# Kernel tuning notes

Measured on AMD Instinct MI355X. Metric: run time of the kernel, lower is better.

## Reference

```python
import jax, jax.numpy as jnp
import numpy as np

HID = 384
KV = 384
HEADS = 2
LAYERS = 2
KFFN = 9
WIN = 0.2
SIGMA = 0.3
EPS = 1e-5
HDIM = HID // HEADS


def _sin_pos(T, dim):
    # fairseq SinusoidalPositionalEmbedding; inputs are nonzero floats so all
    # positions are "non-pad": positions = arange(T) + padding_idx + 1 = 1..T
    pos = jnp.arange(1, T + 1, dtype=jnp.float32)
    half = dim // 2
    freqs = jnp.exp(-np.log(10000.0) / (half - 1) * jnp.arange(half, dtype=jnp.float32))
    ang = pos[:, None] * freqs[None, :]
    return jnp.concatenate([jnp.sin(ang), jnp.cos(ang)], axis=-1)  # [T, dim]


def _ln(x, g, b):
    m = jnp.mean(x, axis=-1, keepdims=True)
    v = jnp.var(x, axis=-1, keepdims=True)
    return (x - m) * jax.lax.rsqrt(v + EPS) * g + b


def _window_mask(T1, T2):
    # per-query sliding window over keys (vectorized form of the Python loop)
    w = int(T2 * WIN) // 2
    t = jnp.arange(T1)
    c = (t * T2) // T1                      # win_center = int(t/T1*T2)
    lo = jnp.maximum(0, c - w)
    j = jnp.arange(T2)
    allowed = (j[None, :] >= lo[:, None]) & (j[None, :] < (c + w)[:, None])
    return ~allowed                          # True = masked out, [T1, T2]


def _forward(x1, x2, pos_alpha, ln1_g, ln1_b, qw, kw, vw, ow,
             ln2_g, ln2_b, cw, cb, lw, lb, lnf_g, lnf_b):
    B, T1, C = x1.shape
    T2 = x2.shape[1]
    # no padding (random-normal inputs never have zero abs-sum rows), so all
    # nonpadding multiplies are identity and key_padding_mask is a no-op.
    x1 = x1 + pos_alpha * _sin_pos(T1, C)[None]
    x2 = x2 + pos_alpha * _sin_pos(T2, KV)[None]

    mask = _window_mask(T1, T2)              # [T1, T2] bool
    scaling = HDIM ** -0.5
    guided_loss = jnp.float32(0.0)
    # guided attention mask (lengths == full lengths, no padding)
    ti = jnp.arange(T1, dtype=jnp.float32)[:, None] / T1
    sj = jnp.arange(T2, dtype=jnp.float32)[None, :] / T2
    gmask = 1.0 - jnp.exp(-((sj - ti) ** 2) / (2.0 * SIGMA ** 2))  # [T1, T2]

    aw = None
    for i in range(LAYERS):
        residual = x1
        qn = _ln(x1, ln1_g[i], ln1_b[i])
        q = jnp.einsum('btc,dc->btd', qn, qw[i]) * scaling
        k = jnp.einsum('bsc,dc->bsd', x2, kw[i])
        v = jnp.einsum('bsc,dc->bsd', x2, vw[i])
        q = q.reshape(B, T1, HEADS, HDIM)
        k = k.reshape(B, T2, HEADS, HDIM)
        v = v.reshape(B, T2, HEADS, HDIM)
        scores = jnp.einsum('bqhd,bkhd->bhqk', q, k)
        scores = jnp.where(mask[None, None], jnp.float32(-1e9), scores)
        p = jax.nn.softmax(scores, axis=-1)                  # [B,H,T1,T2]
        attn = jnp.einsum('bhqk,bkhd->bqhd', p, v).reshape(B, T1, C)
        attn = jnp.einsum('btc,dc->btd', attn, ow[i])
        x1 = residual + attn
        if i == 0:  # num_guided_layers = 1
            aw = p.mean(axis=1)                              # head-avg [B,T1,T2]
            guided_loss = guided_loss + (aw * gmask[None]).mean()
        # FFN: Conv1d(C->4C, k=9, SAME) * k^-0.5 -> gelu -> Linear(4C->C)
        residual = x1
        y = _ln(x1, ln2_g[i], ln2_b[i])
        yt = jnp.transpose(y, (0, 2, 1))                     # [B,C,T1]
        h = jax.lax.conv_general_dilated(yt, cw[i], (1,), 'SAME',
                                         dimension_numbers=('NCH', 'OIH', 'NCH'))
        h = (h + cb[i][None, :, None]) * (KFFN ** -0.5)
        h = jax.nn.gelu(jnp.transpose(h, (0, 2, 1)), approximate=False)  # [B,T1,4C]
        y = jnp.einsum('btf,cf->btc', h, lw[i]) + lb[i]
        x1 = residual + y

    x1 = _ln(x1, lnf_g, lnf_b)
    return x1, guided_loss


def setup_inputs() -> dict:
    key = jax.random.key(0)
    ks = jax.random.split(key, 16)
    s = 0.02
    B, T1, T2 = 8, 2048, 512
    return {
        'x1': jax.random.normal(ks[0], (B, T1, HID), jnp.float32),
        'x2': jax.random.normal(ks[1], (B, T2, KV), jnp.float32),
        'pos_alpha': jnp.float32(1.0),
        'ln1_g': jnp.ones((LAYERS, HID), jnp.float32),
        'ln1_b': jnp.zeros((LAYERS, HID), jnp.float32),
        'qw': jax.random.normal(ks[2], (LAYERS, HID, HID), jnp.float32) * s,
        'kw': jax.random.normal(ks[3], (LAYERS, HID, KV), jnp.float32) * s,
        'vw': jax.random.normal(ks[4], (LAYERS, HID, KV), jnp.float32) * s,
        'ow': jax.random.normal(ks[5], (LAYERS, HID, HID), jnp.float32) * s,
        'ln2_g': jnp.ones((LAYERS, HID), jnp.float32),
        'ln2_b': jnp.zeros((LAYERS, HID), jnp.float32),
        'cw': jax.random.normal(ks[6], (LAYERS, 4 * HID, HID, KFFN), jnp.float32) * s,
        'cb': jnp.zeros((LAYERS, 4 * HID), jnp.float32),
        'lw': jax.random.normal(ks[7], (LAYERS, HID, 4 * HID), jnp.float32) * s,
        'lb': jnp.zeros((LAYERS, HID), jnp.float32),
        'lnf_g': jnp.ones((HID,), jnp.float32),
        'lnf_b': jnp.zeros((HID,), jnp.float32),
    }


def reference(x1, x2, pos_alpha, ln1_g, ln1_b, qw, kw, vw, ow,
              ln2_g, ln2_b, cw, cb, lw, lb, lnf_g, lnf_b):
    return _forward(x1, x2, pos_alpha, ln1_g, ln1_b, qw, kw, vw, ow,
                    ln2_g, ln2_b, cw, cb, lw, lb, lnf_g, lnf_b)
```

## Files before the change

### kernel.cpp

```cpp
#include <hip/hip_runtime.h>
#include <math.h>

#define NB 8
#define NT1 2048
#define NT2 512
#define NC 384
#define ND 192
#define NF 1536
#define NKI 3456
#define TPAD 2056

typedef __attribute__((ext_vector_type(8))) short bf16x8;
typedef __attribute__((ext_vector_type(4))) float f32x4;

#define GLOAD16(gsrc, ldst) \
  __builtin_amdgcn_global_load_lds((const __attribute__((address_space(1))) void*)(gsrc), \
                                   (__attribute__((address_space(3))) void*)(ldst), 16, 0, 0)

static __device__ __forceinline__ unsigned short f2bf(float f) {
  unsigned int u = __float_as_uint(f);
  unsigned int r = (u + 0x7fffu + ((u >> 16) & 1u)) >> 16;
  return (unsigned short)r;
}

static __device__ __forceinline__ float warp_sum(float v) {
#pragma unroll
  for (int off = 32; off > 0; off >>= 1) v += __shfl_xor(v, off);
  return v;
}

__global__ __launch_bounds__(256) void k_add_pos2(const float* __restrict__ x,
    const float* __restrict__ alpha_p, float* __restrict__ y, int T, int total2) {
  int i = blockIdx.x * 256 + threadIdx.x;
  if (i >= total2) return;
  int j = i % 192;
  int row = i / 192;
  int t = row % T;
  float freq = __expf(-0.0482216773f * (float)j);
  float ang = (float)(t + 1) * freq;
  float sn, cs;
  __sincosf(ang, &sn, &cs);
  float a = alpha_p[0];
  size_t base = (size_t)row * NC;
  y[base + j] = x[base + j] + a * sn;
  y[base + j + 192] = x[base + j + 192] + a * cs;
}

__global__ __launch_bounds__(256) void k_add_pos2_bf16(const float* __restrict__ x,
    const float* __restrict__ alpha_p, unsigned short* __restrict__ y, int T, int total2) {
  int i = blockIdx.x * 256 + threadIdx.x;
  if (i >= total2) return;
  int j = i % 192;
  int row = i / 192;
  int t = row % T;
  float freq = __expf(-0.0482216773f * (float)j);
  float ang = (float)(t + 1) * freq;
  float sn, cs;
  __sincosf(ang, &sn, &cs);
  float a = alpha_p[0];
  size_t base = (size_t)row * NC;
  y[base + j] = f2bf(x[base + j] + a * sn);
  y[base + j + 192] = f2bf(x[base + j + 192] + a * cs);
}

__global__ __launch_bounds__(256) void k_ln(const float* __restrict__ x,
    const float* __restrict__ g, const float* __restrict__ b,
    float* __restrict__ y, int nrows) {
  int row = blockIdx.x * 4 + (threadIdx.x >> 6);
  int lane = threadIdx.x & 63;
  if (row >= nrows) return;
  const float* xr = x + (size_t)row * NC;
  float v[6];
  float s = 0.f, s2 = 0.f;
#pragma unroll
  for (int i = 0; i < 6; ++i) {
    float t = xr[lane + 64 * i];
    v[i] = t; s += t; s2 += t * t;
  }
  s = warp_sum(s); s2 = warp_sum(s2);
  float mean = s * (1.f / NC);
  float var = s2 * (1.f / NC) - mean * mean;
  float rs = rsqrtf(var + 1e-5f);
  float* yr = y + (size_t)row * NC;
#pragma unroll
  for (int i = 0; i < 6; ++i) {
    int cc = lane + 64 * i;
    yr[cc] = (v[i] - mean) * rs * g[cc] + b[cc];
  }
}

__global__ __launch_bounds__(256) void k_ln_bf16(const float* __restrict__ x,
    const float* __restrict__ g, const float* __restrict__ b,
    unsigned short* __restrict__ y) {
  int row = blockIdx.x * 4 + (threadIdx.x >> 6);
  int lane = threadIdx.x & 63;
  const float* xr = x + (size_t)row * NC;
  float v[6];
  float s = 0.f, s2 = 0.f;
#pragma unroll
  for (int i = 0; i < 6; ++i) {
    float t = xr[lane + 64 * i];
    v[i] = t; s += t; s2 += t * t;
  }
  s = warp_sum(s); s2 = warp_sum(s2);
  float mean = s * (1.f / NC);
  float var = s2 * (1.f / NC) - mean * mean;
  float rs = rsqrtf(var + 1e-5f);
  unsigned short* yr = y + (size_t)row * NC;
#pragma unroll
  for (int i = 0; i < 6; ++i) {
    int cc = lane + 64 * i;
    yr[cc] = f2bf((v[i] - mean) * rs * g[cc] + b[cc]);
  }
}

__global__ __launch_bounds__(256) void k_ln_bf16p(const float* __restrict__ x,
    const float* __restrict__ g, const float* __restrict__ b,
    unsigned short* __restrict__ ypad) {
  int row = blockIdx.x * 4 + (threadIdx.x >> 6);
  int lane = threadIdx.x & 63;
  const float* xr = x + (size_t)row * NC;
  float v[6];
  float s = 0.f, s2 = 0.f;
#pragma unroll
  for (int i = 0; i < 6; ++i) {
    float t = xr[lane + 64 * i];
    v[i] = t; s += t; s2 += t * t;
  }
  s = warp_sum(s); s2 = warp_sum(s2);
  float mean = s * (1.f / NC);
  float var = s2 * (1.f / NC) - mean * mean;
  float rs = rsqrtf(var + 1e-5f);
  int bb = row >> 11, t = row & 2047;
  unsigned short* yr = ypad + ((size_t)(bb * TPAD + t + 4)) * NC;
#pragma unroll
  for (int i = 0; i < 6; ++i) {
    int cc = lane + 64 * i;
    yr[cc] = f2bf((v[i] - mean) * rs * g[cc] + b[cc]);
  }
}

__global__ __launch_bounds__(256) void k_zero_guard(unsigned short* __restrict__ ypad) {
  int i = blockIdx.x * 256 + threadIdx.x;
  if (i >= 24576) return;
  int c = i % NC;
  int r = (i / NC) % 8;
  int b = i / (NC * 8);
  int t = (r < 4) ? r : (2048 + r);
  ypad[((size_t)b * TPAD + t) * NC + c] = 0;
}

__global__ __launch_bounds__(256) void k_pack_cw2(const float* __restrict__ cw,
    unsigned short* __restrict__ cwp) {
  __shared__ float s[NKI];
  int f = blockIdx.x;
  const float* src = cw + (size_t)f * NKI;
  for (int i = threadIdx.x; i < NKI; i += 256) s[i] = src[i];
  __syncthreads();
  unsigned short* dst = cwp + (size_t)f * NKI;
  for (int i = threadIdx.x; i < NKI; i += 256) {
    int kk = i / NC, cc = i - kk * NC;
    dst[i] = f2bf(s[cc * 9 + kk]);
  }
}

__global__ __launch_bounds__(256) void k_cvt_scale(const float* __restrict__ x,
    unsigned short* __restrict__ y, int n, float scale) {
  int i = blockIdx.x * 256 + threadIdx.x;
  if (i < n) y[i] = f2bf(x[i] * scale);
}

__global__ __launch_bounds__(256) void k_pgemm_mfma(
    const unsigned short* __restrict__ A,
    const unsigned short* __restrict__ W,
    unsigned short* __restrict__ Cb,
    float* __restrict__ Cf,
    int K, int mode) {
  __shared__ unsigned short As[128 * 32];
  __shared__ unsigned short Bs[128 * 32];
  const int bn = blockIdx.x * 128;
  const int bm = blockIdx.y * 128;
  const int tid = threadIdx.x;
  const int lane = tid & 63, wv = tid >> 6;
  const int wr = (wv >> 1) * 64, wc = (wv & 1) * 64;
  f32x4 acc[4][4] = {};

  const int chunk = wv * 2;
  const int rloc = chunk * 16 + (lane >> 2);
  const int slot = (lane & 3) * 8;
  const size_t abase = ((size_t)(bm + rloc)) * K + slot;
  const size_t bbase = ((size_t)(bn + rloc)) * K + slot;
  unsigned short* AsW0 = &As[chunk * 512];
  unsigned short* AsW1 = &As[(chunk + 1) * 512];
  unsigned short* BsW0 = &Bs[chunk * 512];
  unsigned short* BsW1 = &Bs[(chunk + 1) * 512];

  const int rsel = lane & 15, ksel = (lane >> 4) * 8;

  for (int kt = 0; kt < K; kt += 32) {
    GLOAD16(A + abase + kt, AsW0);
    GLOAD16(A + abase + kt + (size_t)16 * K, AsW1);
    GLOAD16(W + bbase + kt, BsW0);
    GLOAD16(W + bbase + kt + (size_t)16 * K, BsW1);
    __syncthreads();
    bf16x8 af[4], bfr[4];
#pragma unroll
    for (int m = 0; m < 4; ++m)
      af[m] = *(const bf16x8*)&As[(wr + m * 16 + rsel) * 32 + ksel];
#pragma unroll
    for (int n = 0; n < 4; ++n)
      bfr[n] = *(const bf16x8*)&Bs[(wc + n * 16 + rsel) * 32 + ksel];
#pragma unroll
    for (int m = 0; m < 4; ++m)
#pragma unroll
      for (int n = 0; n < 4; ++n)
        acc[m][n] = __builtin_amdgcn_mfma_f32_16x16x32_bf16(af[m], bfr[n], acc[m][n], 0, 0, 0);
    __syncthreads();
  }

  const int col0 = bn + wc + (lane & 15);
  const int row0 = bm + wr + (lane >> 4) * 4;
#pragma unroll
  for (int m = 0; m < 4; ++m) {
#pragma unroll
    for (int n = 0; n < 4; ++n) {
      int col = col0 + n * 16;
#pragma unroll
      for (int r = 0; r < 4; ++r) {
        int row = row0 + m * 16 + r;
        if (mode == 0) {
          Cb[(size_t)row * NC + col] = f2bf(acc[m][n][r]);
        } else if (mode == 1) {
          size_t oi = (size_t)row * NC + col;
          Cf[oi] = acc[m][n][r] + Cf[oi];
        } else {
          Cb[((size_t)((row >> 9) * 384 + col)) * 512 + (row & 511)] = f2bf(acc[m][n][r]);
        }
      }
    }
  }
}

__global__ __launch_bounds__(512) void k_conv_mfma(
    const unsigned short* __restrict__ Ypad,
    const unsigned short* __restrict__ Wp,
    const float* __restrict__ cb,
    unsigned short* __restrict__ H) {
  __shared__ unsigned short As[2][256 * 64];
  __shared__ unsigned short Bs[2][128 * 64];
  const int bm = blockIdx.x * 256;
  const int bn = blockIdx.y * 128;
  const int b = bm >> 11, t0 = bm & 2047;
  const int tid = threadIdx.x;
  const int lane = tid & 63, wv = tid >> 6;
  const int wvM = wv >> 1, wvN = wv & 1;
  const int rsel = lane & 15, ghi = lane >> 4;
  const int l8 = lane >> 3, g8 = lane & 7;
  const int gsrc = (g8 ^ l8) * 8;

  f32x4 acc[4][4] = {};

  const size_t arow0 = (size_t)(b * TPAD + t0 + wv * 32 + l8);
  const size_t brow0 = (size_t)(bn + wv * 16 + l8);

#define CONV_STAGE(T, DB)                                                     \
  {                                                                           \
    const int kt_ = (T) * 64;                                                 \
    const int kk_ = kt_ / NC;                                                 \
    const int c0_ = kt_ - kk_ * NC;                                           \
    const size_t asrc_ = (arow0 + kk_) * NC + c0_ + gsrc;                     \
    GLOAD16(Ypad + asrc_, &As[DB][(wv * 32) * 64]);                           \
    GLOAD16(Ypad + asrc_ + (size_t)8 * NC, &As[DB][(wv * 32 + 8) * 64]);      \
    GLOAD16(Ypad + asrc_ + (size_t)16 * NC, &As[DB][(wv * 32 + 16) * 64]);    \
    GLOAD16(Ypad + asrc_ + (size_t)24 * NC, &As[DB][(wv * 32 + 24) * 64]);    \
    const size_t bsrc_ = brow0 * NKI + kt_ + gsrc;                            \
    GLOAD16(Wp + bsrc_, &Bs[DB][(wv * 16) * 64]);                             \
    GLOAD16(Wp + bsrc_ + (size_t)8 * NKI, &Bs[DB][(wv * 16 + 8) * 64]);       \
  }

  CONV_STAGE(0, 0);
  CONV_STAGE(1, 1);
  asm volatile("s_waitcnt vmcnt(6)" ::: "memory");
  __builtin_amdgcn_sched_barrier(0);
  __builtin_amdgcn_s_barrier();

  const int arow = wvM * 64;
  const int brow = wvN * 64;
  int db = 0;
  for (int t = 0; t < 54; ++t) {
    bf16x8 af[4][2], bfr[4][2];
#pragma unroll
    for (int m = 0; m < 4; ++m) {
      int r = arow + m * 16 + rsel;
#pragma unroll
      for (int k = 0; k < 2; ++k)
        af[m][k] = *(const bf16x8*)&As[db][r * 64 + (((k * 4 + ghi) ^ (r & 7)) * 8)];
    }
#pragma unroll
    for (int n = 0; n < 4; ++n) {
      int r = brow + n * 16 + rsel;
#pragma unroll
      for (int k = 0; k < 2; ++k)
        bfr[n][k] = *(const bf16x8*)&Bs[db][r * 64 + (((k * 4 + ghi) ^ (r & 7)) * 8)];
    }
    __builtin_amdgcn_s_setprio(1);
#pragma unroll
    for (int m = 0; m < 4; ++m)
#pragma unroll
      for (int n = 0; n < 4; ++n)
        acc[m][n] = __builtin_amdgcn_mfma_f32_16x16x32_bf16(af[m][0], bfr[n][0], acc[m][n], 0, 0, 0);
    __builtin_amdgcn_s_setprio(0);
    __builtin_amdgcn_sched_barrier(0);
    asm volatile("s_waitcnt lgkmcnt(0)" ::: "memory");
    __builtin_amdgcn_sched_barrier(0);
    __builtin_amdgcn_s_barrier();
    if (t + 2 < 54) CONV_STAGE(t + 2, db);
    __builtin_amdgcn_s_setprio(1);
#pragma unroll
    for (int m = 0; m < 4; ++m)
#pragma unroll
      for (int n = 0; n < 4; ++n)
        acc[m][n] = __builtin_amdgcn_mfma_f32_16x16x32_bf16(af[m][1], bfr[n][1], acc[m][n], 0, 0, 0);
    __builtin_amdgcn_s_setprio(0);
    __builtin_amdgcn_sched_barrier(0);
    if (t + 2 < 54) {
      asm volatile("s_waitcnt vmcnt(6)" ::: "memory");
    } else {
      asm volatile("s_waitcnt vmcnt(0)" ::: "memory");
    }
    __builtin_amdgcn_sched_barrier(0);
    __builtin_amdgcn_s_barrier();
    db ^= 1;
  }
#undef CONV_STAGE

  const int col0 = bn + wvN * 64 + rsel;
  const int row0 = bm + wvM * 64 + ghi * 4;
#pragma unroll
  for (int m = 0; m < 4; ++m) {
#pragma unroll
    for (int n = 0; n < 4; ++n) {
      int col = col0 + n * 16;
      float cbv = cb[col];
#pragma unroll
      for (int r = 0; r < 4; ++r) {
        int row = row0 + m * 16 + r;
        float xv = (acc[m][n][r] + cbv) * 0.33333333333333333f;
        float ge = 0.5f * xv * (1.f + erff(xv * 0.70710678118654752f));
        H[(size_t)row * NF + col] = f2bf(ge);
      }
    }
  }
}

__global__ __launch_bounds__(256) void k_lin_mfma(
    const unsigned short* __restrict__ H,
    const unsigned short* __restrict__ Wb,
    const float* __restrict__ lb,
    float* __restrict__ x1a) {
  __shared__ unsigned short As[128 * 32];
  __shared__ unsigned short Bs[128 * 32];
  const int bn = blockIdx.x * 128;
  const int bm = blockIdx.y * 128;
  const int tid = threadIdx.x;
  const int lane = tid & 63, wv = tid >> 6;
  const int wr = (wv >> 1) * 64, wc = (wv & 1) * 64;
  f32x4 acc[4][4] = {};

  const int chunk = wv * 2;
  const int rloc = chunk * 16 + (lane >> 2);
  const int slot = (lane & 3) * 8;
  const size_t abase = ((size_t)(bm + rloc)) * NF + slot;
  const size_t bbase = ((size_t)(bn + rloc)) * NF + slot;
  unsigned short* AsW0 = &As[chunk * 512];
  unsigned short* AsW1 = &As[(chunk + 1) * 512];
  unsigned short* BsW0 = &Bs[chunk * 512];
  unsigned short* BsW1 = &Bs[(chunk + 1) * 512];

  const int rsel = lane & 15, ksel = (lane >> 4) * 8;

  for (int kt = 0; kt < NF; kt += 32) {
    GLOAD16(H + abase + kt, AsW0);
    GLOAD16(H + abase + kt + (size_t)16 * NF, AsW1);
    GLOAD16(Wb + bbase + kt, BsW0);
    GLOAD16(Wb + bbase + kt + (size_t)16 * NF, BsW1);
    __syncthreads();
    bf16x8 af[4], bfr[4];
#pragma unroll
    for (int m = 0; m < 4; ++m)
      af[m] = *(const bf16x8*)&As[(wr + m * 16 + rsel) * 32 + ksel];
#pragma unroll
    for (int n = 0; n < 4; ++n)
      bfr[n] = *(const bf16x8*)&Bs[(wc + n * 16 + rsel) * 32 + ksel];
#pragma unroll
    for (int m = 0; m < 4; ++m)
#pragma unroll
      for (int n = 0; n < 4; ++n)
        acc[m][n] = __builtin_amdgcn_mfma_f32_16x16x32_bf16(af[m], bfr[n], acc[m][n], 0, 0, 0);
    __syncthreads();
  }

  const int col0 = bn + wc + (lane & 15);
  const int row0 = bm + wr + (lane >> 4) * 4;
#pragma unroll
  for (int m = 0; m < 4; ++m) {
#pragma unroll
    for (int n = 0; n < 4; ++n) {
      int col = col0 + n * 16;
      float lbv = lb[col];
#pragma unroll
      for (int r = 0; r < 4; ++r) {
        int row = row0 + m * 16 + r;
        size_t oi = (size_t)row * NC + col;
        x1a[oi] = acc[m][n][r] + lbv + x1a[oi];
      }
    }
  }
}

__global__ __launch_bounds__(256) void k_attn_mfma(
    const unsigned short* __restrict__ qbb,
    const unsigned short* __restrict__ kbb,
    const unsigned short* __restrict__ vtb,
    unsigned short* __restrict__ o, int guided, float* __restrict__ gl) {
  __shared__ unsigned short lds[32768];
  const int tid = threadIdx.x;
  const int lane = tid & 63, wv = tid >> 6;
  const int rsel = lane & 15, ghi = lane >> 4;
  const int idx = blockIdx.x;
  const int tg = idx & 31;
  const int bh = idx >> 5;
  const int h = bh & 1, b = bh >> 1;
  const int t0 = tg * 64;
  const int c0 = t0 >> 2;
  int klo = c0 - 51; if (klo < 0) klo = 0;
  klo &= ~7;
  if (klo > 384) klo = 384;

  const unsigned short* qrow = qbb + (size_t)(b * NT1 + t0 + wv * 16 + rsel) * NC + h * ND;
  bf16x8 qf[6];
#pragma unroll
  for (int kk = 0; kk < 6; ++kk)
    qf[kk] = *(const bf16x8*)(qrow + kk * 32 + ghi * 8);

  {
    const size_t kbase = (size_t)(b * NT2 + klo) * NC + h * ND;
#pragma unroll
    for (int it = 0; it < 12; ++it) {
      int g = it * 256 + tid;
      int row = g / 24, go = g % 24;
      int gs = go ^ (row & 7);
      GLOAD16(kbb + kbase + (size_t)row * NC + gs * 8, &lds[(it * 256 + wv * 64) * 8]);
    }
  }
  __syncthreads();

  f32x4 accs[8] = {};
#pragma unroll
  for (int kk = 0; kk < 6; ++kk) {
#pragma unroll
    for (int n = 0; n < 8; ++n) {
      int row = n * 16 + rsel;
      bf16x8 bfr = *(const bf16x8*)&lds[row * 192 + (((kk * 4 + ghi) ^ (rsel & 7)) * 8)];
      accs[n] = __builtin_amdgcn_mfma_f32_16x16x32_bf16(qf[kk], bfr, accs[n], 0, 0, 0);
    }
  }

  unsigned short* pl = &lds[24576 + wv * 2048];
  float gacc = 0.f;
  const int t0w = t0 + wv * 16;
#pragma unroll
  for (int r = 0; r < 4; ++r) {
    int t = t0w + ghi * 4 + r;
    int c = t >> 2;
    int loq = c - 51; if (loq < 0) loq = 0;
    int hiq = c + 51; if (hiq > NT2) hiq = NT2;
    float sv[8];
    float mx = -1e30f;
#pragma unroll
    for (int n = 0; n < 8; ++n) {
      int j = klo + n * 16 + rsel;
      float s = (j >= loq && j < hiq) ? accs[n][r] : -1e30f;
      sv[n] = s; mx = fmaxf(mx, s);
    }
#pragma unroll
    for (int off = 1; off < 16; off <<= 1) mx = fmaxf(mx, __shfl_xor(mx, off));
    float e[8]; float se = 0.f;
#pragma unroll
    for (int n = 0; n < 8; ++n) { e[n] = __expf(sv[n] - mx); se += e[n]; }
#pragma unroll
    for (int off = 1; off < 16; off <<= 1) se += __shfl_xor(se, off);
    float inv = 1.f / se;
    int q = ghi * 4 + r;
#pragma unroll
    for (int n = 0; n < 8; ++n) {
      float pv = e[n] * inv;
      int klocal = n * 16 + rsel;
      pl[q * 128 + (((klocal >> 3) ^ (q & 7)) * 8) + (klocal & 7)] = f2bf(pv);
      if (guided) {
        int j = klo + klocal;
        float d = (float)j * (1.f / NT2) - (float)t * (1.f / NT1);
        gacc += pv * (1.f - __expf(-(d * d) * 5.5555555556f));
      }
    }
  }
  if (guided) {
    gacc = warp_sum(gacc);
    if (lane == 0) atomicAdd(gl, gacc * (1.f / 16777216.f));
  }
  __syncthreads();

  {
    const size_t vbase = ((size_t)(b * 2 + h) * ND) * NT2 + klo;
#pragma unroll
    for (int it = 0; it < 12; ++it) {
      int g = it * 256 + tid;
      int row = g >> 4, go = g & 15;
      int gs = go ^ (row & 7);
      GLOAD16(vtb + vbase + (size_t)row * NT2 + gs * 8, &lds[(it * 256 + wv * 64) * 8]);
    }
  }
  __syncthreads();

  f32x4 acco[12] = {};
#pragma unroll
  for (int kt = 0; kt < 4; ++kt) {
    bf16x8 pa = *(const bf16x8*)&pl[rsel * 128 + (((kt * 4 + ghi) ^ (rsel & 7)) * 8)];
#pragma unroll
    for (int n = 0; n < 12; ++n) {
      int row = n * 16 + rsel;
      bf16x8 bfr = *(const bf16x8*)&lds[row * 128 + (((kt * 4 + ghi) ^ (rsel & 7)) * 8)];
      acco[n] = __builtin_amdgcn_mfma_f32_16x16x32_bf16(pa, bfr, acco[n], 0, 0, 0);
    }
  }

  unsigned short* obase = o + (size_t)(b * NT1 + t0w + ghi * 4) * NC + h * ND;
#pragma unroll
  for (int n = 0; n < 12; ++n) {
#pragma unroll
    for (int r = 0; r < 4; ++r) {
      obase[(size_t)r * NC + n * 16 + rsel] = f2bf(acco[n][r]);
    }
  }
}

extern "C" void kernel_launch(void* const* d_in, const int* in_sizes, int n_in,
                              void* d_out, int out_size, void* d_ws, size_t ws_size,
                              hipStream_t stream) {
  (void)in_sizes; (void)n_in; (void)out_size; (void)ws_size;
  const float* x1    = (const float*)d_in[0];
  const float* x2    = (const float*)d_in[1];
  const float* alpha = (const float*)d_in[2];
  const float* ln1_g = (const float*)d_in[3];
  const float* ln1_b = (const float*)d_in[4];
  const float* qw    = (const float*)d_in[5];
  const float* kw    = (const float*)d_in[6];
  const float* vw    = (const float*)d_in[7];
  const float* ow    = (const float*)d_in[8];
  const float* ln2_g = (const float*)d_in[9];
  const float* ln2_b = (const float*)d_in[10];
  const float* cw    = (const float*)d_in[11];
  const float* cb    = (const float*)d_in[12];
  const float* lw    = (const float*)d_in[13];
  const float* lb    = (const float*)d_in[14];
  const float* lnf_g = (const float*)d_in[15];
  const float* lnf_b = (const float*)d_in[16];
  float* out = (float*)d_out;
  float* gl = out + 6291456;

  float* p = (float*)d_ws;
  float* x1a = p; p += 6291456;
  unsigned short* us = (unsigned short*)p;
  unsigned short* x2b  = us; us += 1572864;
  unsigned short* tmpb = us; us += 6291456;
  unsigned short* ypad = us; us += 8 * TPAD * NC;
  unsigned short* cwpb = us; us += 2 * (size_t)NF * NKI;
  unsigned short* lwb  = us; us += 2 * (size_t)NC * NF;
  unsigned short* hb   = us; us += (size_t)16384 * NF;
  unsigned short* qbb  = us; us += 6291456;
  unsigned short* kbb  = us; us += 1572864;
  unsigned short* vtb  = us; us += 1572864;
  unsigned short* qwb  = us; us += 294912;
  unsigned short* kwb  = us; us += 294912;
  unsigned short* vwb  = us; us += 294912;
  unsigned short* owb  = us; us += 294912;

  hipMemsetAsync(gl, 0, sizeof(float), stream);
  k_zero_guard<<<96, 256, 0, stream>>>(ypad);
  k_add_pos2<<<12288, 256, 0, stream>>>(x1, alpha, x1a, NT1, 3145728);
  k_add_pos2_bf16<<<3072, 256, 0, stream>>>(x2, alpha, x2b, NT2, 786432);

  const float scaling = 0.07216878364870323f;
  k_cvt_scale<<<1152, 256, 0, stream>>>(qw, qwb, 294912, scaling);
  k_cvt_scale<<<1152, 256, 0, stream>>>(kw, kwb, 294912, 1.f);
  k_cvt_scale<<<1152, 256, 0, stream>>>(vw, vwb, 294912, 1.f);
  k_cvt_scale<<<1152, 256, 0, stream>>>(ow, owb, 294912, 1.f);
  k_cvt_scale<<<4608, 256, 0, stream>>>(lw, lwb, 1179648, 1.f);
  k_pack_cw2<<<3072, 256, 0, stream>>>(cw, cwpb);

  for (int l = 0; l < 2; ++l) {
    k_ln_bf16<<<4096, 256, 0, stream>>>(x1a, ln1_g + l * 384, ln1_b + l * 384, tmpb);
    k_pgemm_mfma<<<dim3(3, 128), 256, 0, stream>>>(tmpb, qwb + (size_t)l * 147456, qbb, nullptr, 384, 0);
    k_pgemm_mfma<<<dim3(3, 32), 256, 0, stream>>>(x2b, kwb + (size_t)l * 147456, kbb, nullptr, 384, 0);
    k_pgemm_mfma<<<dim3(3, 32), 256, 0, stream>>>(x2b, vwb + (size_t)l * 147456, vtb, nullptr, 384, 2);
    k_attn_mfma<<<512, 256, 0, stream>>>(qbb, kbb, vtb, tmpb, l == 0 ? 1 : 0, gl);
    k_pgemm_mfma<<<dim3(3, 128), 256, 0, stream>>>(tmpb, owb + (size_t)l * 147456, nullptr, x1a, 384, 1);
    k_ln_bf16p<<<4096, 256, 0, stream>>>(x1a, ln2_g + l * 384, ln2_b + l * 384, ypad);
    k_conv_mfma<<<dim3(64, 12), 512, 0, stream>>>(ypad, cwpb + (size_t)l * 5308416, cb + l * 1536, hb);
    k_lin_mfma<<<dim3(3, 128), 256, 0, stream>>>(hb, lwb + (size_t)l * 589824, lb + l * 384, x1a);
  }
  k_ln<<<4096, 256, 0, stream>>>(x1a, lnf_g, lnf_b, out, 16384);
}
```

Before: 750.8 us.

## Enlarge conv GEMM tile to 256x256 with swizzled block order and split fragment loads

Changes the conv MFMA kernel's block tile from 256x128 to 256x256, with each wave computing a 128x64 sub-tile (8x4 accumulators), so each loaded A and B element is reused more often. The 1D grid of 384 blocks is remapped with a swizzle that groups blocks sharing the same A rows, aiming at better L2 reuse. Second-half LDS fragment loads are now issued after the first MFMA batch to overlap them with compute. LDS use and register pressure roughly double, so occupancy may drop, and launch_bounds(512,2) may force spills.

```diff
diff --git a/kernel.cpp b/kernel.cpp
--- a/kernel.cpp
+++ b/kernel.cpp
@@ -241,27 +241,29 @@
   }
 }
 
-__global__ __launch_bounds__(512) void k_conv_mfma(
+__global__ __launch_bounds__(512, 2) void k_conv_mfma(
     const unsigned short* __restrict__ Ypad,
     const unsigned short* __restrict__ Wp,
     const float* __restrict__ cb,
     unsigned short* __restrict__ H) {
   __shared__ unsigned short As[2][256 * 64];
-  __shared__ unsigned short Bs[2][128 * 64];
-  const int bm = blockIdx.x * 256;
-  const int bn = blockIdx.y * 128;
+  __shared__ unsigned short Bs[2][256 * 64];
+  const int id = blockIdx.x;
+  const int swz = (id & 7) * 48 + (id >> 3);
+  const int bm = (swz % 64) * 256;
+  const int bn = (swz / 64) * 256;
   const int b = bm >> 11, t0 = bm & 2047;
   const int tid = threadIdx.x;
   const int lane = tid & 63, wv = tid >> 6;
-  const int wvM = wv >> 1, wvN = wv & 1;
+  const int wvM = wv >> 2, wvN = wv & 3;
   const int rsel = lane & 15, ghi = lane >> 4;
   const int l8 = lane >> 3, g8 = lane & 7;
   const int gsrc = (g8 ^ l8) * 8;
 
-  f32x4 acc[4][4] = {};
+  f32x4 acc[8][4] = {};
 
   const size_t arow0 = (size_t)(b * TPAD + t0 + wv * 32 + l8);
-  const size_t brow0 = (size_t)(bn + wv * 16 + l8);
+  const size_t brow0 = (size_t)(bn + wv * 32 + l8);
 
 #define CONV_STAGE(T, DB)                                                     \
   {                                                                           \
@@ -274,57 +276,65 @@
     GLOAD16(Ypad + asrc_ + (size_t)16 * NC, &As[DB][(wv * 32 + 16) * 64]);    \
     GLOAD16(Ypad + asrc_ + (size_t)24 * NC, &As[DB][(wv * 32 + 24) * 64]);    \
     const size_t bsrc_ = brow0 * NKI + kt_ + gsrc;                            \
-    GLOAD16(Wp + bsrc_, &Bs[DB][(wv * 16) * 64]);                             \
-    GLOAD16(Wp + bsrc_ + (size_t)8 * NKI, &Bs[DB][(wv * 16 + 8) * 64]);       \
+    GLOAD16(Wp + bsrc_, &Bs[DB][(wv * 32) * 64]);                             \
+    GLOAD16(Wp + bsrc_ + (size_t)8 * NKI, &Bs[DB][(wv * 32 + 8) * 64]);       \
+    GLOAD16(Wp + bsrc_ + (size_t)16 * NKI, &Bs[DB][(wv * 32 + 16) * 64]);     \
+    GLOAD16(Wp + bsrc_ + (size_t)24 * NKI, &Bs[DB][(wv * 32 + 24) * 64]);     \
   }
 
   CONV_STAGE(0, 0);
   CONV_STAGE(1, 1);
-  asm volatile("s_waitcnt vmcnt(6)" ::: "memory");
+  asm volatile("s_waitcnt vmcnt(8)" ::: "memory");
   __builtin_amdgcn_sched_barrier(0);
   __builtin_amdgcn_s_barrier();
 
-  const int arow = wvM * 64;
+  const int arow = wvM * 128;
   const int brow = wvN * 64;
   int db = 0;
   for (int t = 0; t < 54; ++t) {
-    bf16x8 af[4][2], bfr[4][2];
-#pragma unroll
-    for (int m = 0; m < 4; ++m) {
+    bf16x8 a0[8], b0[4];
+#pragma unroll
+    for (int m = 0; m < 8; ++m) {
       int r = arow + m * 16 + rsel;
-#pragma unroll
-      for (int k = 0; k < 2; ++k)
-        af[m][k] = *(const bf16x8*)&As[db][r * 64 + (((k * 4 + ghi) ^ (r & 7)) * 8)];
+      a0[m] = *(const bf16x8*)&As[db][r * 64 + ((ghi ^ (r & 7)) * 8)];
     }
 #pragma unroll
     for (int n = 0; n < 4; ++n) {
       int r = brow + n * 16 + rsel;
-#pragma unroll
-      for (int k = 0; k < 2; ++k)
-        bfr[n][k] = *(const bf16x8*)&Bs[db][r * 64 + (((k * 4 + ghi) ^ (r & 7)) * 8)];
+      b0[n] = *(const bf16x8*)&Bs[db][r * 64 + ((ghi ^ (r & 7)) * 8)];
     }
     __builtin_amdgcn_s_setprio(1);
 #pragma unroll
-    for (int m = 0; m < 4; ++m)
+    for (int m = 0; m < 8; ++m)
 #pragma unroll
       for (int n = 0; n < 4; ++n)
-        acc[m][n] = __builtin_amdgcn_mfma_f32_16x16x32_bf16(af[m][0], bfr[n][0], acc[m][n], 0, 0, 0);
+        acc[m][n] = __builtin_amdgcn_mfma_f32_16x16x32_bf16(a0[m], b0[n], acc[m][n], 0, 0, 0);
     __builtin_amdgcn_s_setprio(0);
-    __builtin_amdgcn_sched_barrier(0);
+    bf16x8 a1[8], b1[4];
+#pragma unroll
+    for (int m = 0; m < 8; ++m) {
+      int r = arow + m * 16 + rsel;
+      a1[m] = *(const bf16x8*)&As[db][r * 64 + (((4 + ghi) ^ (r & 7)) * 8)];
+    }
+#pragma unroll
+    for (int n = 0; n < 4; ++n) {
+      int r = brow + n * 16 + rsel;
+      b1[n] = *(const bf16x8*)&Bs[db][r * 64 + (((4 + ghi) ^ (r & 7)) * 8)];
+    }
     asm volatile("s_waitcnt lgkmcnt(0)" ::: "memory");
     __builtin_amdgcn_sched_barrier(0);
     __builtin_amdgcn_s_barrier();
     if (t + 2 < 54) CONV_STAGE(t + 2, db);
     __builtin_amdgcn_s_setprio(1);
 #pragma unroll
-    for (int m = 0; m < 4; ++m)
+    for (int m = 0; m < 8; ++m)
 #pragma unroll
       for (int n = 0; n < 4; ++n)
-        acc[m][n] = __builtin_amdgcn_mfma_f32_16x16x32_bf16(af[m][1], bfr[n][1], acc[m][n], 0, 0, 0);
+        acc[m][n] = __builtin_amdgcn_mfma_f32_16x16x32_bf16(a1[m], b1[n], acc[m][n], 0, 0, 0);
     __builtin_amdgcn_s_setprio(0);
     __builtin_amdgcn_sched_barrier(0);
     if (t + 2 < 54) {
-      asm volatile("s_waitcnt vmcnt(6)" ::: "memory");
+      asm volatile("s_waitcnt vmcnt(8)" ::: "memory");
     } else {
       asm volatile("s_waitcnt vmcnt(0)" ::: "memory");
     }
@@ -335,9 +345,9 @@
 #undef CONV_STAGE
 
   const int col0 = bn + wvN * 64 + rsel;
-  const int row0 = bm + wvM * 64 + ghi * 4;
-#pragma unroll
-  for (int m = 0; m < 4; ++m) {
+  const int row0 = bm + wvM * 128 + ghi * 4;
+#pragma unroll
+  for (int m = 0; m < 8; ++m) {
 #pragma unroll
     for (int n = 0; n < 4; ++n) {
       int col = col0 + n * 16;
@@ -606,7 +616,7 @@
     k_attn_mfma<<<512, 256, 0, stream>>>(qbb, kbb, vtb, tmpb, l == 0 ? 1 : 0, gl);
     k_pgemm_mfma<<<dim3(3, 128), 256, 0, stream>>>(tmpb, owb + (size_t)l * 147456, nullptr, x1a, 384, 1);
     k_ln_bf16p<<<4096, 256, 0, stream>>>(x1a, ln2_g + l * 384, ln2_b + l * 384, ypad);
-    k_conv_mfma<<<dim3(64, 12), 512, 0, stream>>>(ypad, cwpb + (size_t)l * 5308416, cb + l * 1536, hb);
+    k_conv_mfma<<<384, 512, 0, stream>>>(ypad, cwpb + (size_t)l * 5308416, cb + l * 1536, hb);
     k_lin_mfma<<<dim3(3, 128), 256, 0, stream>>>(hb, lwb + (size_t)l * 589824, lb + l * 384, x1a);
   }
   k_ln<<<4096, 256, 0, stream>>>(x1a, lnf_g, lnf_b, out, 16384);
```

New measurement: 792.6 us. +5.6%, slower.

## Triple-buffer conv GEMM pipeline and merge small conversion and K/V launches

Applied to the files above, without the earlier changes.

The conv MFMA kernel moves from a double-buffered LDS pipeline to three buffers. It issues the load for stage t+2 before computing stage t, so each iteration needs one barrier pair instead of splitting the MFMAs around the prefetch. The four QKVO weight conversions become one launch, and the K and V projection GEMMs become one launch using a z-dimension. The intent is more memory latency hiding in the dominant conv kernel and fewer launches. In exchange the conv kernel uses 1.5x the LDS, which may reduce occupancy, and the s_setprio hints are dropped.

```diff
diff --git a/kernel.cpp b/kernel.cpp
--- a/kernel.cpp
+++ b/kernel.cpp
@@ -164,10 +164,22 @@
   }
 }
 
-__global__ __launch_bounds__(256) void k_cvt_scale(const float* __restrict__ x,
-    unsigned short* __restrict__ y, int n, float scale) {
+__global__ __launch_bounds__(256) void k_cvt_qkvo(const float* __restrict__ qw,
+    const float* __restrict__ kw, const float* __restrict__ vw,
+    const float* __restrict__ ow, unsigned short* __restrict__ dst, float qscale) {
   int i = blockIdx.x * 256 + threadIdx.x;
-  if (i < n) y[i] = f2bf(x[i] * scale);
+  if (i >= 4 * 294912) return;
+  int w = i / 294912;
+  int j = i - w * 294912;
+  const float* s = (w == 0) ? qw : (w == 1) ? kw : (w == 2) ? vw : ow;
+  float sc = (w == 0) ? qscale : 1.f;
+  dst[i] = f2bf(s[j] * sc);
+}
+
+__global__ __launch_bounds__(256) void k_cvt(const float* __restrict__ x,
+    unsigned short* __restrict__ y, int n) {
+  int i = blockIdx.x * 256 + threadIdx.x;
+  if (i < n) y[i] = f2bf(x[i]);
 }
 
 __global__ __launch_bounds__(256) void k_pgemm_mfma(
@@ -230,11 +242,79 @@
         int row = row0 + m * 16 + r;
         if (mode == 0) {
           Cb[(size_t)row * NC + col] = f2bf(acc[m][n][r]);
-        } else if (mode == 1) {
+        } else {
           size_t oi = (size_t)row * NC + col;
           Cf[oi] = acc[m][n][r] + Cf[oi];
+        }
+      }
+    }
+  }
+}
+
+__global__ __launch_bounds__(256) void k_pgemm_kv(
+    const unsigned short* __restrict__ A,
+    const unsigned short* __restrict__ Wk,
+    const unsigned short* __restrict__ Wv,
+    unsigned short* __restrict__ Kb,
+    unsigned short* __restrict__ Vtb) {
+  __shared__ unsigned short As[128 * 32];
+  __shared__ unsigned short Bs[128 * 32];
+  const int z = blockIdx.z;
+  const unsigned short* W = z ? Wv : Wk;
+  const int bn = blockIdx.x * 128;
+  const int bm = blockIdx.y * 128;
+  const int tid = threadIdx.x;
+  const int lane = tid & 63, wv = tid >> 6;
+  const int wr = (wv >> 1) * 64, wc = (wv & 1) * 64;
+  f32x4 acc[4][4] = {};
+
+  const int chunk = wv * 2;
+  const int rloc = chunk * 16 + (lane >> 2);
+  const int slot = (lane & 3) * 8;
+  const size_t abase = ((size_t)(bm + rloc)) * NC + slot;
+  const size_t bbase = ((size_t)(bn + rloc)) * NC + slot;
+  unsigned short* AsW0 = &As[chunk * 512];
+  unsigned short* AsW1 = &As[(chunk + 1) * 512];
+  unsigned short* BsW0 = &Bs[chunk * 512];
+  unsigned short* BsW1 = &Bs[(chunk + 1) * 512];
+
+  const int rsel = lane & 15, ksel = (lane >> 4) * 8;
+
+  for (int kt = 0; kt < NC; kt += 32) {
+    GLOAD16(A + abase + kt, AsW0);
+    GLOAD16(A + abase + kt + (size_t)16 * NC, AsW1);
+    GLOAD16(W + bbase + kt, BsW0);
+    GLOAD16(W + bbase + kt + (size_t)16 * NC, BsW1);
+    __syncthreads();
+    bf16x8 af[4], bfr[4];
+#pragma unroll
+    for (int m = 0; m < 4; ++m)
+      af[m] = *(const bf16x8*)&As[(wr + m * 16 + rsel) * 32 + ksel];
+#pragma unroll
+    for (int n = 0; n < 4; ++n)
+      bfr[n] = *(const bf16x8*)&Bs[(wc + n * 16 + rsel) * 32 + ksel];
+#pragma unroll
+    for (int m = 0; m < 4; ++m)
+#pragma unroll
+      for (int n = 0; n < 4; ++n)
+        acc[m][n] = __builtin_amdgcn_mfma_f32_16x16x32_bf16(af[m], bfr[n], acc[m][n], 0, 0, 0);
+    __syncthreads();
+  }
+
+  const int col0 = bn + wc + (lane & 15);
+  const int row0 = bm + wr + (lane >> 4) * 4;
+#pragma unroll
+  for (int m = 0; m < 4; ++m) {
+#pragma unroll
+    for (int n = 0; n < 4; ++n) {
+      int col = col0 + n * 16;
+#pragma unroll
+      for (int r = 0; r < 4; ++r) {
+        int row = row0 + m * 16 + r;
+        if (z == 0) {
+          Kb[(size_t)row * NC + col] = f2bf(acc[m][n][r]);
         } else {
-          Cb[((size_t)((row >> 9) * 384 + col)) * 512 + (row & 511)] = f2bf(acc[m][n][r]);
+          Vtb[((size_t)((row >> 9) * 384 + col)) * 512 + (row & 511)] = f2bf(acc[m][n][r]);
         }
       }
     }
@@ -246,8 +326,8 @@
     const unsigned short* __restrict__ Wp,
     const float* __restrict__ cb,
     unsigned short* __restrict__ H) {
-  __shared__ unsigned short As[2][256 * 64];
-  __shared__ unsigned short Bs[2][128 * 64];
+  __shared__ unsigned short As[3][256 * 64];
+  __shared__ unsigned short Bs[3][128 * 64];
   const int bm = blockIdx.x * 256;
   const int bn = blockIdx.y * 128;
   const int b = bm >> 11, t0 = bm & 2047;
@@ -263,19 +343,61 @@
   const size_t arow0 = (size_t)(b * TPAD + t0 + wv * 32 + l8);
   const size_t brow0 = (size_t)(bn + wv * 16 + l8);
 
-#define CONV_STAGE(T, DB)                                                     \
+#define CONV_STAGE(T, RB)                                                     \
   {                                                                           \
     const int kt_ = (T) * 64;                                                 \
     const int kk_ = kt_ / NC;                                                 \
     const int c0_ = kt_ - kk_ * NC;                                           \
     const size_t asrc_ = (arow0 + kk_) * NC + c0_ + gsrc;                     \
-    GLOAD16(Ypad + asrc_, &As[DB][(wv * 32) * 64]);                           \
-    GLOAD16(Ypad + asrc_ + (size_t)8 * NC, &As[DB][(wv * 32 + 8) * 64]);      \
-    GLOAD16(Ypad + asrc_ + (size_t)16 * NC, &As[DB][(wv * 32 + 16) * 64]);    \
-    GLOAD16(Ypad + asrc_ + (size_t)24 * NC, &As[DB][(wv * 32 + 24) * 64]);    \
+    GLOAD16(Ypad + asrc_, &As[RB][(wv * 32) * 64]);                           \
+    GLOAD16(Ypad + asrc_ + (size_t)8 * NC, &As[RB][(wv * 32 + 8) * 64]);      \
+    GLOAD16(Ypad + asrc_ + (size_t)16 * NC, &As[RB][(wv * 32 + 16) * 64]);    \
+    GLOAD16(Ypad + asrc_ + (size_t)24 * NC, &As[RB][(wv * 32 + 24) * 64]);    \
     const size_t bsrc_ = brow0 * NKI + kt_ + gsrc;                            \
-    GLOAD16(Wp + bsrc_, &Bs[DB][(wv * 16) * 64]);                             \
-    GLOAD16(Wp + bsrc_ + (size_t)8 * NKI, &Bs[DB][(wv * 16 + 8) * 64]);       \
+    GLOAD16(Wp + bsrc_, &Bs[RB][(wv * 16) * 64]);                             \
+    GLOAD16(Wp + bsrc_ + (size_t)8 * NKI, &Bs[RB][(wv * 16 + 8) * 64]);       \
+  }
+
+  const int arow = wvM * 64;
+  const int brow = wvN * 64;
+
+#define CONV_ITER(T, RC, RS)                                                  \
+  {                                                                           \
+    if ((T) + 2 < 54) {                                                       \
+      CONV_STAGE((T) + 2, RS);                                                \
+      asm volatile("s_waitcnt vmcnt(12)" ::: "memory");                       \
+    } else if ((T) + 1 < 54) {                                                \
+      asm volatile("s_waitcnt vmcnt(6)" ::: "memory");                        \
+    } else {                                                                  \
+      asm volatile("s_waitcnt vmcnt(0)" ::: "memory");                        \
+    }                                                                         \
+    __builtin_amdgcn_sched_barrier(0);                                        \
+    __builtin_amdgcn_s_barrier();           \
+    bf16x8 af[4][2], bfr[4][2];                                               \
+    _Pragma("unroll")                                                         \
+    for (int m = 0; m < 4; ++m) {                                             \
+      int r = arow + m * 16 + rsel;                                           \
+      _Pragma("unroll")                                                       \
+      for (int k = 0; k < 2; ++k)                                             \
+        af[m][k] = *(const bf16x8*)&As[RC][r * 64 + (((k * 4 + ghi) ^ (r & 7)) * 8)]; \
+    }                                                                         \
+    _Pragma("unroll")                                                         \
+    for (int n = 0; n < 4; ++n) {                                             \
+      int r = brow + n * 16 + rsel;                                           \
+      _Pragma("unroll")                                                       \
+      for (int k = 0; k < 2; ++k)                                             \
+        bfr[n][k] = *(const bf16x8*)&Bs[RC][r * 64 + (((k * 4 + ghi) ^ (r & 7)) * 8)]; \
+    }                                                                         \
+    _Pragma("unroll")                                                         \
+    for (int k = 0; k < 2; ++k)                                               \
+      _Pragma("unroll")                                                       \
+      for (int m = 0; m < 4; ++m)                                             \
+        _Pragma("unroll")                                                     \
+        for (int n = 0; n < 4; ++n)                                           \
+          acc[m][n] = __builtin_amdgcn_mfma_f32_16x16x32_bf16(af[m][k], bfr[n][k], acc[m][n], 0, 0, 0); \
+    asm volatile("s_waitcnt lgkmcnt(0)" ::: "memory");   \
+    __builtin_amdgcn_sched_barrier(0);                                        \
+    __builtin_amdgcn_s_barrier();               \
   }
 
   CONV_STAGE(0, 0);
@@ -284,54 +406,12 @@
   __builtin_amdgcn_sched_barrier(0);
   __builtin_amdgcn_s_barrier();
 
-  const int arow = wvM * 64;
-  const int brow = wvN * 64;
-  int db = 0;
-  for (int t = 0; t < 54; ++t) {
-    bf16x8 af[4][2], bfr[4][2];
-#pragma unroll
-    for (int m = 0; m < 4; ++m) {
-      int r = arow + m * 16 + rsel;
-#pragma unroll
-      for (int k = 0; k < 2; ++k)
-        af[m][k] = *(const bf16x8*)&As[db][r * 64 + (((k * 4 + ghi) ^ (r & 7)) * 8)];
-    }
-#pragma unroll
-    for (int n = 0; n < 4; ++n) {
-      int r = brow + n * 16 + rsel;
-#pragma unroll
-      for (int k = 0; k < 2; ++k)
-        bfr[n][k] = *(const bf16x8*)&Bs[db][r * 64 + (((k * 4 + ghi) ^ (r & 7)) * 8)];
-    }
-    __builtin_amdgcn_s_setprio(1);
-#pragma unroll
-    for (int m = 0; m < 4; ++m)
-#pragma unroll
-      for (int n = 0; n < 4; ++n)
-        acc[m][n] = __builtin_amdgcn_mfma_f32_16x16x32_bf16(af[m][0], bfr[n][0], acc[m][n], 0, 0, 0);
-    __builtin_amdgcn_s_setprio(0);
-    __builtin_amdgcn_sched_barrier(0);
-    asm volatile("s_waitcnt lgkmcnt(0)" ::: "memory");
-    __builtin_amdgcn_sched_barrier(0);
-    __builtin_amdgcn_s_barrier();
-    if (t + 2 < 54) CONV_STAGE(t + 2, db);
-    __builtin_amdgcn_s_setprio(1);
-#pragma unroll
-    for (int m = 0; m < 4; ++m)
-#pragma unroll
-      for (int n = 0; n < 4; ++n)
-        acc[m][n] = __builtin_amdgcn_mfma_f32_16x16x32_bf16(af[m][1], bfr[n][1], acc[m][n], 0, 0, 0);
-    __builtin_amdgcn_s_setprio(0);
-    __builtin_amdgcn_sched_barrier(0);
-    if (t + 2 < 54) {
-      asm volatile("s_waitcnt vmcnt(6)" ::: "memory");
-    } else {
-      asm volatile("s_waitcnt vmcnt(0)" ::: "memory");
-    }
-    __builtin_amdgcn_sched_barrier(0);
-    __builtin_amdgcn_s_barrier();
-    db ^= 1;
-  }
+  for (int t3 = 0; t3 < 54; t3 += 3) {
+    CONV_ITER(t3 + 0, 0, 2);
+    CONV_ITER(t3 + 1, 1, 0);
+    CONV_ITER(t3 + 2, 2, 1);
+  }
+#undef CONV_ITER
 #undef CONV_STAGE
 
   const int col0 = bn + wvN * 64 + rsel;
@@ -591,18 +671,15 @@
   k_add_pos2_bf16<<<3072, 256, 0, stream>>>(x2, alpha, x2b, NT2, 786432);
 
   const float scaling = 0.07216878364870323f;
-  k_cvt_scale<<<1152, 256, 0, stream>>>(qw, qwb, 294912, scaling);
-  k_cvt_scale<<<1152, 256, 0, stream>>>(kw, kwb, 294912, 1.f);
-  k_cvt_scale<<<1152, 256, 0, stream>>>(vw, vwb, 294912, 1.f);
-  k_cvt_scale<<<1152, 256, 0, stream>>>(ow, owb, 294912, 1.f);
-  k_cvt_scale<<<4608, 256, 0, stream>>>(lw, lwb, 1179648, 1.f);
+  k_cvt_qkvo<<<4608, 256, 0, stream>>>(qw, kw, vw, ow, qwb, scaling);
+  k_cvt<<<4608, 256, 0, stream>>>(lw, lwb, 1179648);
   k_pack_cw2<<<3072, 256, 0, stream>>>(cw, cwpb);
 
   for (int l = 0; l < 2; ++l) {
     k_ln_bf16<<<4096, 256, 0, stream>>>(x1a, ln1_g + l * 384, ln1_b + l * 384, tmpb);
     k_pgemm_mfma<<<dim3(3, 128), 256, 0, stream>>>(tmpb, qwb + (size_t)l * 147456, qbb, nullptr, 384, 0);
-    k_pgemm_mfma<<<dim3(3, 32), 256, 0, stream>>>(x2b, kwb + (size_t)l * 147456, kbb, nullptr, 384, 0);
-    k_pgemm_mfma<<<dim3(3, 32), 256, 0, stream>>>(x2b, vwb + (size_t)l * 147456, vtb, nullptr, 384, 2);
+    k_pgemm_kv<<<dim3(3, 32, 2), 256, 0, stream>>>(x2b, kwb + (size_t)l * 147456,
+                                                   vwb + (size_t)l * 147456, kbb, vtb);
     k_attn_mfma<<<512, 256, 0, stream>>>(qbb, kbb, vtb, tmpb, l == 0 ? 1 : 0, gl);
     k_pgemm_mfma<<<dim3(3, 128), 256, 0, stream>>>(tmpb, owb + (size_t)l * 147456, nullptr, x1a, 384, 1);
     k_ln_bf16p<<<4096, 256, 0, stream>>>(x1a, ln2_g + l * 384, ln2_b + l * 384, ypad);
```

Result: slower. 778.3 us (+3.7%).
